# Kernel optimization log

Measured on AMD Instinct MI355X. Metric: run time of the kernel, lower is better.

## Reference

```python
import jax, jax.numpy as jnp
import numpy as np

DIM = 768
NUM_HEADS = 12
HEAD_DIM = DIM // NUM_HEADS
SCALE = HEAD_DIM ** -0.5


def setup_inputs() -> dict:
    key = jax.random.key(0)
    k_x, k_qkv, k_proj, k_pb = jax.random.split(key, 4)
    B, N, C = 16, 1024, DIM
    x = jax.random.normal(k_x, (B, N, C), dtype=jnp.float32)
    # qkv Linear: weight [3C, C], no bias (qkv_bias=False)
    w_qkv = jax.random.normal(k_qkv, (3 * C, C), dtype=jnp.float32) * (C ** -0.5)
    # proj Linear: weight [C, C], bias [C]
    w_proj = jax.random.normal(k_proj, (C, C), dtype=jnp.float32) * (C ** -0.5)
    b_proj = jax.random.normal(k_pb, (C,), dtype=jnp.float32) * 0.01
    return {"x": x, "w_qkv": w_qkv, "w_proj": w_proj, "b_proj": b_proj}


def reference(x, w_qkv, w_proj, b_proj):
    B, N, C = x.shape
    H, D = NUM_HEADS, HEAD_DIM
    # qkv projection: [B,N,3C] -> [3,B,H,N,D]
    qkv = jnp.einsum('bnc,ec->bne', x, w_qkv)
    qkv = qkv.reshape(B, N, 3, H, D).transpose(2, 0, 3, 1, 4)
    q, k, v = qkv[0], qkv[1], qkv[2]
    # manual attention: scores [B,H,N,N] materialized, as in source
    attn = jnp.einsum('bhqd,bhkd->bhqk', q, k) * SCALE
    attn = jax.nn.softmax(attn, axis=-1)
    out = jnp.einsum('bhqk,bhkd->bhqd', attn, v)  # [B,H,N,D]
    out = out.transpose(0, 2, 1, 3).reshape(B, N, C)
    out = jnp.einsum('bnc,oc->bno', out, w_proj) + b_proj
    return out
```

## Files before the change

kernel.cpp:

```cpp
#include <hip/hip_runtime.h>
#include <hip/hip_bf16.h>
#include <stdint.h>

typedef __attribute__((ext_vector_type(8))) short short8;
typedef __attribute__((ext_vector_type(4))) short short4v;
typedef __attribute__((ext_vector_type(4))) float floatx4;

#define B_   16
#define N_   1024
#define C_   768
#define H_   12
#define D_   64
#define K_   768
#define QSCALE 0.18033688011112042f

__device__ __forceinline__ short f2bf(float f) {
    __hip_bfloat16 h = __float2bfloat16(f);
    short s; __builtin_memcpy(&s, &h, 2); return s;
}
__device__ __forceinline__ unsigned pk2bf(float a, float b) {
    __hip_bfloat162 h = __float22bfloat162_rn(make_float2(a, b));
    unsigned u; __builtin_memcpy(&u, &h, 4); return u;
}

__device__ __forceinline__ void gl_lds16(const void* g, void* l) {
    __builtin_amdgcn_global_load_lds(
        (const __attribute__((address_space(1))) unsigned int*)g,
        (__attribute__((address_space(3))) unsigned int*)l, 16, 0, 0);
}

#define N8_X  1572864
#define N8_WQ 221184
#define N8_WP 73728
__global__ void cvt_all(const float* __restrict__ x, const float* __restrict__ wq,
                        const float* __restrict__ wp, short* __restrict__ xb,
                        short* __restrict__ wqb, short* __restrict__ wpb)
{
    long i = (long)blockIdx.x * 256 + threadIdx.x;
    const float* src; short* dst;
    if (i < N8_X)              { src = x;  dst = xb;  }
    else if (i < N8_X + N8_WQ) { src = wq; dst = wqb; i -= N8_X; }
    else                       { src = wp; dst = wpb; i -= (long)N8_X + N8_WQ; }
    const float4* p = (const float4*)src + 2 * i;
    const float4 u = p[0], v = p[1];
    short8 r;
    r[0] = f2bf(u.x); r[1] = f2bf(u.y); r[2] = f2bf(u.z); r[3] = f2bf(u.w);
    r[4] = f2bf(v.x); r[5] = f2bf(v.y); r[6] = f2bf(v.z); r[7] = f2bf(v.w);
    *((short8*)dst + i) = r;
}

template<int MODE>
__global__ __launch_bounds__(256, 3)
void gemm_bt(const short* __restrict__ A, const short* __restrict__ Bm,
             const float* __restrict__ bias,
             short* __restrict__ q_ws, short* __restrict__ k_ws,
             short* __restrict__ v_ws, float* __restrict__ outp)
{
    __shared__ short Alds[128 * 32];
    __shared__ short Blds[128 * 32];
    const int tid  = threadIdx.x;
    const int wave = tid >> 6, lane = tid & 63;
    const int cl   = lane & 15, quad = lane >> 4;
    const int bm = blockIdx.x, bn = blockIdx.y;
    const int wm = (wave >> 1) * 64, wn = (wave & 1) * 64;

    const short* Ag = A  + (long)bm * 128 * K_ + (long)(tid >> 2) * K_ + (tid & 3) * 8;
    const short* Bg = Bm + (long)bn * 128 * K_ + (long)(tid >> 2) * K_ + (tid & 3) * 8;
    short* la = Alds + (tid & 0xC0) * 8;
    short* lb = Blds + (tid & 0xC0) * 8;

    const floatx4 fzero = {0.f, 0.f, 0.f, 0.f};
    floatx4 acc[4][4];
    #pragma unroll
    for (int i = 0; i < 4; i++)
        #pragma unroll
        for (int j = 0; j < 4; j++) acc[i][j] = fzero;

    for (int kt = 0; kt < K_; kt += 32) {
        __syncthreads();
        gl_lds16(Ag + kt,            la);
        gl_lds16(Ag + kt + 64 * K_,  la + 2048);
        gl_lds16(Bg + kt,            lb);
        gl_lds16(Bg + kt + 64 * K_,  lb + 2048);
        __syncthreads();

        short8 af[4], bf[4];
        #pragma unroll
        for (int i = 0; i < 4; i++)
            af[i] = *(const short8*)(Alds + (wm + i * 16 + cl) * 32 + quad * 8);
        #pragma unroll
        for (int j = 0; j < 4; j++)
            bf[j] = *(const short8*)(Blds + (wn + j * 16 + cl) * 32 + quad * 8);
        #pragma unroll
        for (int i = 0; i < 4; i++)
            #pragma unroll
            for (int j = 0; j < 4; j++)
                acc[i][j] = __builtin_amdgcn_mfma_f32_16x16x32_bf16(af[i], bf[j], acc[i][j], 0, 0, 0);
    }

    #pragma unroll
    for (int i = 0; i < 4; i++) {
        const int gm0 = bm * 128 + wm + i * 16 + quad * 4;
        #pragma unroll
        for (int j = 0; j < 4; j++) {
            const int gn = bn * 128 + wn + j * 16 + cl;
            if (MODE == 0) {
                const int t   = bn / 6;
                const int rem = gn - t * 768;
                const int h   = rem >> 6, d = rem & 63;
                const int b   = gm0 >> 10;
                const int n0  = gm0 & 1023;
                const int bh  = b * H_ + h;
                if (t == 2) {
                    short4v pk;
                    #pragma unroll
                    for (int r = 0; r < 4; r++) pk[r] = f2bf(acc[i][j][r]);
                    *(short4v*)(v_ws + (((long)(bh * D_ + d)) << 10) + n0) = pk;
                } else {
                    short* dst = (t == 0) ? q_ws : k_ws;
                    const float sc = (t == 0) ? QSCALE : 1.0f;
                    #pragma unroll
                    for (int r = 0; r < 4; r++)
                        dst[((long)bh * N_ + (n0 + r)) * D_ + d] = f2bf(acc[i][j][r] * sc);
                }
            } else {
                const float bv = bias[gn];
                #pragma unroll
                for (int r = 0; r < 4; r++)
                    outp[(long)(gm0 + r) * C_ + gn] = acc[i][j][r] + bv;
            }
        }
    }
}

__global__ __launch_bounds__(256, 3)
void attn_fused(const short* __restrict__ q_ws, const short* __restrict__ k_ws,
                const short* __restrict__ v_ws, short* __restrict__ o_ws)
{
    __shared__ short Klds[128 * 72];
    __shared__ short Vlds[64 * 136];
    __shared__ short Plds[4][16 * 136];

    const int tid  = threadIdx.x;
    const int wave = tid >> 6, lane = tid & 63;
    const int cl   = lane & 15, quad = lane >> 4;

    const int linear = blockIdx.y * 8 + blockIdx.x;
    const int xcd = linear & 7, slot = linear >> 3;
    const int bh  = xcd * 24 + (slot >> 3);
    const int qt  = slot & 7;

    const long base = (long)bh * (N_ * D_);
    const int  qr0  = qt * 128 + wave * 32 + cl;

    short8 qf[2][2];
    #pragma unroll
    for (int mt = 0; mt < 2; mt++) {
        qf[mt][0] = *(const short8*)(q_ws + base + (long)(qr0 + mt * 16) * D_ + quad * 8);
        qf[mt][1] = *(const short8*)(q_ws + base + (long)(qr0 + mt * 16) * D_ + 32 + quad * 8);
    }

    const floatx4 fzero = {0.f, 0.f, 0.f, 0.f};
    float m_r[2][4], l_r[2][4];
    floatx4 o_acc[2][4];
    #pragma unroll
    for (int mt = 0; mt < 2; mt++)
        #pragma unroll
        for (int r = 0; r < 4; r++) {
            m_r[mt][r] = -1e30f; l_r[mt][r] = 0.f; o_acc[mt][r] = fzero;
        }

    const int skey = tid >> 3, sseg = (tid & 7) * 8;
    const int vd   = tid >> 4, vc = tid & 15;
    short* pl = &Plds[wave][0];

    for (int kc = 0; kc < N_; kc += 128) {
        short8 kst[4], vst[4];
        #pragma unroll
        for (int p = 0; p < 4; p++) {
            kst[p] = *(const short8*)(k_ws + base + (long)(kc + p * 32 + skey) * D_ + sseg);
            #pragma unroll
            for (int i = 0; i < 8; i++)
                vst[p][i] = v_ws[base + (long)(p * 16 + vd) * N_ + kc + i * 16 + vc];
        }
        __syncthreads();
        #pragma unroll
        for (int p = 0; p < 4; p++) {
            *(short8*)(Klds + (p * 32 + skey) * 72 + sseg) = kst[p];
            *(short8*)(Vlds + (p * 16 + vd) * 136 + vc * 8) = vst[p];
        }
        __syncthreads();

        #pragma unroll
        for (int mt = 0; mt < 2; mt++) {
            floatx4 s[8];
            #pragma unroll
            for (int nt = 0; nt < 8; nt++) {
                short8 kf0 = *(const short8*)(Klds + (nt * 16 + cl) * 72 + quad * 8);
                short8 kf1 = *(const short8*)(Klds + (nt * 16 + cl) * 72 + 32 + quad * 8);
                floatx4 t4 = fzero;
                t4 = __builtin_amdgcn_mfma_f32_16x16x32_bf16(qf[mt][0], kf0, t4, 0, 0, 0);
                t4 = __builtin_amdgcn_mfma_f32_16x16x32_bf16(qf[mt][1], kf1, t4, 0, 0, 0);
                s[nt] = t4;
            }

            float alpha[4];
            #pragma unroll
            for (int r = 0; r < 4; r++) {
                float v = s[0][r];
                #pragma unroll
                for (int nt = 1; nt < 8; nt++) v = fmaxf(v, s[nt][r]);
                v = fmaxf(v, __shfl_xor(v, 1));
                v = fmaxf(v, __shfl_xor(v, 2));
                v = fmaxf(v, __shfl_xor(v, 4));
                v = fmaxf(v, __shfl_xor(v, 8));
                const float mn = fmaxf(m_r[mt][r], v);
                alpha[r] = __builtin_amdgcn_exp2f(m_r[mt][r] - mn);
                m_r[mt][r] = mn;
                l_r[mt][r] *= alpha[r];
            }
            #pragma unroll
            for (int r = 0; r < 4; r++) {
                float p0 = __builtin_amdgcn_exp2f(s[0][r] - m_r[mt][r]);
                float p1 = __builtin_amdgcn_exp2f(s[1][r] - m_r[mt][r]);
                float p2 = __builtin_amdgcn_exp2f(s[2][r] - m_r[mt][r]);
                float p3 = __builtin_amdgcn_exp2f(s[3][r] - m_r[mt][r]);
                float p4 = __builtin_amdgcn_exp2f(s[4][r] - m_r[mt][r]);
                float p5 = __builtin_amdgcn_exp2f(s[5][r] - m_r[mt][r]);
                float p6 = __builtin_amdgcn_exp2f(s[6][r] - m_r[mt][r]);
                float p7 = __builtin_amdgcn_exp2f(s[7][r] - m_r[mt][r]);
                l_r[mt][r] += ((p0 + p1) + (p2 + p3)) + ((p4 + p5) + (p6 + p7));
                uint4 pk = { pk2bf(p0, p1), pk2bf(p2, p3), pk2bf(p4, p5), pk2bf(p6, p7) };
                *(uint4*)(pl + (quad * 4 + r) * 136 + cl * 8) = pk;
            }
            #pragma unroll
            for (int dt = 0; dt < 4; dt++) {
                o_acc[mt][dt][0] *= alpha[0]; o_acc[mt][dt][1] *= alpha[1];
                o_acc[mt][dt][2] *= alpha[2]; o_acc[mt][dt][3] *= alpha[3];
            }
            asm volatile("" ::: "memory");

            #pragma unroll
            for (int ks = 0; ks < 4; ks++) {
                short8 pf = *(const short8*)(pl + cl * 136 + ks * 32 + quad * 8);
                #pragma unroll
                for (int dt = 0; dt < 4; dt++) {
                    short8 vf = *(const short8*)(Vlds + (dt * 16 + cl) * 136 + ks * 32 + quad * 8);
                    o_acc[mt][dt] = __builtin_amdgcn_mfma_f32_16x16x32_bf16(pf, vf, o_acc[mt][dt], 0, 0, 0);
                }
            }
            asm volatile("" ::: "memory");
        }
    }

    const int b = bh / H_, h = bh - b * H_;
    #pragma unroll
    for (int mt = 0; mt < 2; mt++) {
        #pragma unroll
        for (int r = 0; r < 4; r++) {
            float v = l_r[mt][r];
            v += __shfl_xor(v, 1); v += __shfl_xor(v, 2);
            v += __shfl_xor(v, 4); v += __shfl_xor(v, 8);
            l_r[mt][r] = 1.0f / v;
        }
        const int nrow = qt * 128 + wave * 32 + mt * 16 + quad * 4;
        #pragma unroll
        for (int dt = 0; dt < 4; dt++) {
            const int c = h * D_ + dt * 16 + cl;
            #pragma unroll
            for (int r = 0; r < 4; r++)
                o_ws[((long)(b * N_ + nrow + r)) * C_ + c] = f2bf(o_acc[mt][dt][r] * l_r[mt][r]);
        }
    }
}

extern "C" void kernel_launch(void* const* d_in, const int* in_sizes, int n_in,
                              void* d_out, int out_size, void* d_ws, size_t ws_size,
                              hipStream_t stream)
{
    const float* x      = (const float*)d_in[0];
    const float* w_qkv  = (const float*)d_in[1];
    const float* w_proj = (const float*)d_in[2];
    const float* b_proj = (const float*)d_in[3];
    float* out = (float*)d_out;

    const long SZ = (long)B_ * N_ * C_;
    short* q_ws   = (short*)d_ws;
    short* k_ws   = q_ws + SZ;
    short* v_ws   = k_ws + SZ;
    short* x_bf   = v_ws + SZ;
    short* o_ws   = x_bf;
    short* wqkv_bf  = x_bf + SZ;
    short* wproj_bf = wqkv_bf + (long)3 * C_ * C_;

    cvt_all<<<dim3(7296), 256, 0, stream>>>(x, w_qkv, w_proj, x_bf, wqkv_bf, wproj_bf);
    gemm_bt<0><<<dim3(128, 18), 256, 0, stream>>>(x_bf, wqkv_bf, nullptr, q_ws, k_ws, v_ws, nullptr);
    attn_fused<<<dim3(8, 192), 256, 0, stream>>>(q_ws, k_ws, v_ws, o_ws);
    gemm_bt<1><<<dim3(128, 6), 256, 0, stream>>>(o_ws, wproj_bf, b_proj, nullptr, nullptr, nullptr, out);
}
```

Before: 313.2 us.

## Shrink attention KV tile to 64, swizzle LDS, and permute V workspace layout

```diff
diff --git a/kernel.cpp b/kernel.cpp
--- a/kernel.cpp
+++ b/kernel.cpp
@@ -112,10 +112,12 @@
                 const int n0  = gm0 & 1023;
                 const int bh  = b * H_ + h;
                 if (t == 2) {
-                    short4v pk;
                     #pragma unroll
-                    for (int r = 0; r < 4; r++) pk[r] = f2bf(acc[i][j][r]);
-                    *(short4v*)(v_ws + (((long)(bh * D_ + d)) << 10) + n0) = pk;
+                    for (int r = 0; r < 4; r++) {
+                        const int n = n0 + r, w = n & 63;
+                        const int vn = (n & ~63) | (((w & 15) << 2) | (w >> 4));
+                        v_ws[(((long)(bh * D_ + d)) << 10) + vn] = f2bf(acc[i][j][r]);
+                    }
                 } else {
                     short* dst = (t == 0) ? q_ws : k_ws;
                     const float sc = (t == 0) ? QSCALE : 1.0f;
@@ -133,13 +135,13 @@
     }
 }
 
-__global__ __launch_bounds__(256, 3)
+__global__ __launch_bounds__(256, 6)
 void attn_fused(const short* __restrict__ q_ws, const short* __restrict__ k_ws,
                 const short* __restrict__ v_ws, short* __restrict__ o_ws)
 {
-    __shared__ short Klds[128 * 72];
-    __shared__ short Vlds[64 * 136];
-    __shared__ short Plds[4][16 * 136];
+    __shared__ short Klds[64 * 64];
+    __shared__ short Vlds[64 * 64];
+    __shared__ short Plds[4][16 * 72];
 
     const int tid  = threadIdx.x;
     const int wave = tid >> 6, lane = tid & 63;
@@ -170,34 +172,32 @@
             m_r[mt][r] = -1e30f; l_r[mt][r] = 0.f; o_acc[mt][r] = fzero;
         }
 
-    const int skey = tid >> 3, sseg = (tid & 7) * 8;
-    const int vd   = tid >> 4, vc = tid & 15;
+    const int srow = tid >> 2;
+    const int sg0  = (tid & 3) * 2;
+    const int xw   = srow & 7;
+    const int xr   = cl & 7;
     short* pl = &Plds[wave][0];
 
-    for (int kc = 0; kc < N_; kc += 128) {
-        short8 kst[4], vst[4];
-        #pragma unroll
-        for (int p = 0; p < 4; p++) {
-            kst[p] = *(const short8*)(k_ws + base + (long)(kc + p * 32 + skey) * D_ + sseg);
-            #pragma unroll
-            for (int i = 0; i < 8; i++)
-                vst[p][i] = v_ws[base + (long)(p * 16 + vd) * N_ + kc + i * 16 + vc];
-        }
-        __syncthreads();
-        #pragma unroll
-        for (int p = 0; p < 4; p++) {
-            *(short8*)(Klds + (p * 32 + skey) * 72 + sseg) = kst[p];
-            *(short8*)(Vlds + (p * 16 + vd) * 136 + vc * 8) = vst[p];
-        }
+    for (int kc = 0; kc < N_; kc += 64) {
+        short8 k0 = *(const short8*)(k_ws + base + (long)(kc + srow) * D_ + sg0 * 8);
+        short8 k1 = *(const short8*)(k_ws + base + (long)(kc + srow) * D_ + sg0 * 8 + 8);
+        short8 v0 = *(const short8*)(v_ws + base + (long)srow * N_ + kc + sg0 * 8);
+        short8 v1 = *(const short8*)(v_ws + base + (long)srow * N_ + kc + sg0 * 8 + 8);
+        __syncthreads();
+        *(short8*)(Klds + srow * 64 + ((sg0    ) ^ xw) * 8) = k0;
+        *(short8*)(Klds + srow * 64 + ((sg0 + 1) ^ xw) * 8) = k1;
+        *(short8*)(Vlds + srow * 64 + ((sg0    ) ^ xw) * 8) = v0;
+        *(short8*)(Vlds + srow * 64 + ((sg0 + 1) ^ xw) * 8) = v1;
         __syncthreads();
 
         #pragma unroll
         for (int mt = 0; mt < 2; mt++) {
-            floatx4 s[8];
-            #pragma unroll
-            for (int nt = 0; nt < 8; nt++) {
-                short8 kf0 = *(const short8*)(Klds + (nt * 16 + cl) * 72 + quad * 8);
-                short8 kf1 = *(const short8*)(Klds + (nt * 16 + cl) * 72 + 32 + quad * 8);
+            floatx4 s[4];
+            #pragma unroll
+            for (int nt = 0; nt < 4; nt++) {
+                const short* kr = Klds + (nt * 16 + cl) * 64;
+                short8 kf0 = *(const short8*)(kr + ((quad    ) ^ xr) * 8);
+                short8 kf1 = *(const short8*)(kr + ((quad + 4) ^ xr) * 8);
                 floatx4 t4 = fzero;
                 t4 = __builtin_amdgcn_mfma_f32_16x16x32_bf16(qf[mt][0], kf0, t4, 0, 0, 0);
                 t4 = __builtin_amdgcn_mfma_f32_16x16x32_bf16(qf[mt][1], kf1, t4, 0, 0, 0);
@@ -207,9 +207,7 @@
             float alpha[4];
             #pragma unroll
             for (int r = 0; r < 4; r++) {
-                float v = s[0][r];
-                #pragma unroll
-                for (int nt = 1; nt < 8; nt++) v = fmaxf(v, s[nt][r]);
+                float v = fmaxf(fmaxf(s[0][r], s[1][r]), fmaxf(s[2][r], s[3][r]));
                 v = fmaxf(v, __shfl_xor(v, 1));
                 v = fmaxf(v, __shfl_xor(v, 2));
                 v = fmaxf(v, __shfl_xor(v, 4));
@@ -225,13 +223,9 @@
                 float p1 = __builtin_amdgcn_exp2f(s[1][r] - m_r[mt][r]);
                 float p2 = __builtin_amdgcn_exp2f(s[2][r] - m_r[mt][r]);
                 float p3 = __builtin_amdgcn_exp2f(s[3][r] - m_r[mt][r]);
-                float p4 = __builtin_amdgcn_exp2f(s[4][r] - m_r[mt][r]);
-                float p5 = __builtin_amdgcn_exp2f(s[5][r] - m_r[mt][r]);
-                float p6 = __builtin_amdgcn_exp2f(s[6][r] - m_r[mt][r]);
-                float p7 = __builtin_amdgcn_exp2f(s[7][r] - m_r[mt][r]);
-                l_r[mt][r] += ((p0 + p1) + (p2 + p3)) + ((p4 + p5) + (p6 + p7));
-                uint4 pk = { pk2bf(p0, p1), pk2bf(p2, p3), pk2bf(p4, p5), pk2bf(p6, p7) };
-                *(uint4*)(pl + (quad * 4 + r) * 136 + cl * 8) = pk;
+                l_r[mt][r] += (p0 + p1) + (p2 + p3);
+                uint2 pk = { pk2bf(p0, p1), pk2bf(p2, p3) };
+                *(uint2*)(pl + (quad * 4 + r) * 72 + cl * 4) = pk;
             }
             #pragma unroll
             for (int dt = 0; dt < 4; dt++) {
@@ -241,11 +235,12 @@
             asm volatile("" ::: "memory");
 
             #pragma unroll
-            for (int ks = 0; ks < 4; ks++) {
-                short8 pf = *(const short8*)(pl + cl * 136 + ks * 32 + quad * 8);
+            for (int ks = 0; ks < 2; ks++) {
+                short8 pf = *(const short8*)(pl + cl * 72 + ks * 32 + quad * 8);
                 #pragma unroll
                 for (int dt = 0; dt < 4; dt++) {
-                    short8 vf = *(const short8*)(Vlds + (dt * 16 + cl) * 136 + ks * 32 + quad * 8);
+                    const short* vr = Vlds + (dt * 16 + cl) * 64;
+                    short8 vf = *(const short8*)(vr + ((ks * 4 + quad) ^ xr) * 8);
                     o_acc[mt][dt] = __builtin_amdgcn_mfma_f32_16x16x32_bf16(pf, vf, o_acc[mt][dt], 0, 0, 0);
                 }
             }
```

Result: slower. 459.8 us (+46.8%).

## Vectorize V loads, XOR-swizzle K/V LDS, share K fragments across row tiles

Applied to the files above, without the earlier changes.

```diff
diff --git a/kernel.cpp b/kernel.cpp
--- a/kernel.cpp
+++ b/kernel.cpp
@@ -137,8 +137,8 @@
 void attn_fused(const short* __restrict__ q_ws, const short* __restrict__ k_ws,
                 const short* __restrict__ v_ws, short* __restrict__ o_ws)
 {
-    __shared__ short Klds[128 * 72];
-    __shared__ short Vlds[64 * 136];
+    __shared__ short Klds[128 * 64];
+    __shared__ short Vlds[64 * 128];
     __shared__ short Plds[4][16 * 136];
 
     const int tid  = threadIdx.x;
@@ -170,46 +170,51 @@
             m_r[mt][r] = -1e30f; l_r[mt][r] = 0.f; o_acc[mt][r] = fzero;
         }
 
-    const int skey = tid >> 3, sseg = (tid & 7) * 8;
-    const int vd   = tid >> 4, vc = tid & 15;
+    const int skey = tid >> 3, sseg = tid & 7;
+    const int vd   = tid >> 4, vseg = tid & 15;
     short* pl = &Plds[wave][0];
 
     for (int kc = 0; kc < N_; kc += 128) {
         short8 kst[4], vst[4];
         #pragma unroll
         for (int p = 0; p < 4; p++) {
-            kst[p] = *(const short8*)(k_ws + base + (long)(kc + p * 32 + skey) * D_ + sseg);
-            #pragma unroll
-            for (int i = 0; i < 8; i++)
-                vst[p][i] = v_ws[base + (long)(p * 16 + vd) * N_ + kc + i * 16 + vc];
+            kst[p] = *(const short8*)(k_ws + base + (long)(kc + p * 32 + skey) * D_ + sseg * 8);
+            vst[p] = *(const short8*)(v_ws + base + (long)(p * 16 + vd) * N_ + kc + vseg * 8);
         }
         __syncthreads();
         #pragma unroll
         for (int p = 0; p < 4; p++) {
-            *(short8*)(Klds + (p * 32 + skey) * 72 + sseg) = kst[p];
-            *(short8*)(Vlds + (p * 16 + vd) * 136 + vc * 8) = vst[p];
+            const int krow = p * 32 + skey;
+            const int fk   = ((krow >> 3) ^ (krow & 7)) & 7;
+            *(short8*)(Klds + krow * 64 + (sseg ^ fk) * 8) = kst[p];
+            const int vrow = p * 16 + vd;
+            *(short8*)(Vlds + vrow * 128 + (vseg ^ (vrow & 7)) * 8) = vst[p];
         }
         __syncthreads();
 
+        floatx4 s[2][8];
+        #pragma unroll
+        for (int nt = 0; nt < 8; nt++) {
+            const int krow = cl * 8 + nt;
+            const int fk   = ((krow >> 3) ^ (krow & 7)) & 7;
+            const short* kr = Klds + krow * 64;
+            short8 kf0 = *(const short8*)(kr + ((quad    ) ^ fk) * 8);
+            short8 kf1 = *(const short8*)(kr + ((quad + 4) ^ fk) * 8);
+            floatx4 t0 = fzero, t1 = fzero;
+            t0 = __builtin_amdgcn_mfma_f32_16x16x32_bf16(qf[0][0], kf0, t0, 0, 0, 0);
+            t0 = __builtin_amdgcn_mfma_f32_16x16x32_bf16(qf[0][1], kf1, t0, 0, 0, 0);
+            t1 = __builtin_amdgcn_mfma_f32_16x16x32_bf16(qf[1][0], kf0, t1, 0, 0, 0);
+            t1 = __builtin_amdgcn_mfma_f32_16x16x32_bf16(qf[1][1], kf1, t1, 0, 0, 0);
+            s[0][nt] = t0; s[1][nt] = t1;
+        }
+
         #pragma unroll
         for (int mt = 0; mt < 2; mt++) {
-            floatx4 s[8];
-            #pragma unroll
-            for (int nt = 0; nt < 8; nt++) {
-                short8 kf0 = *(const short8*)(Klds + (nt * 16 + cl) * 72 + quad * 8);
-                short8 kf1 = *(const short8*)(Klds + (nt * 16 + cl) * 72 + 32 + quad * 8);
-                floatx4 t4 = fzero;
-                t4 = __builtin_amdgcn_mfma_f32_16x16x32_bf16(qf[mt][0], kf0, t4, 0, 0, 0);
-                t4 = __builtin_amdgcn_mfma_f32_16x16x32_bf16(qf[mt][1], kf1, t4, 0, 0, 0);
-                s[nt] = t4;
-            }
-
             float alpha[4];
             #pragma unroll
             for (int r = 0; r < 4; r++) {
-                float v = s[0][r];
-                #pragma unroll
-                for (int nt = 1; nt < 8; nt++) v = fmaxf(v, s[nt][r]);
+                float v = fmaxf(fmaxf(s[mt][0][r], s[mt][1][r]), fmaxf(s[mt][2][r], s[mt][3][r]));
+                v = fmaxf(v, fmaxf(fmaxf(s[mt][4][r], s[mt][5][r]), fmaxf(s[mt][6][r], s[mt][7][r])));
                 v = fmaxf(v, __shfl_xor(v, 1));
                 v = fmaxf(v, __shfl_xor(v, 2));
                 v = fmaxf(v, __shfl_xor(v, 4));
@@ -221,14 +226,14 @@
             }
             #pragma unroll
             for (int r = 0; r < 4; r++) {
-                float p0 = __builtin_amdgcn_exp2f(s[0][r] - m_r[mt][r]);
-                float p1 = __builtin_amdgcn_exp2f(s[1][r] - m_r[mt][r]);
-                float p2 = __builtin_amdgcn_exp2f(s[2][r] - m_r[mt][r]);
-                float p3 = __builtin_amdgcn_exp2f(s[3][r] - m_r[mt][r]);
-                float p4 = __builtin_amdgcn_exp2f(s[4][r] - m_r[mt][r]);
-                float p5 = __builtin_amdgcn_exp2f(s[5][r] - m_r[mt][r]);
-                float p6 = __builtin_amdgcn_exp2f(s[6][r] - m_r[mt][r]);
-                float p7 = __builtin_amdgcn_exp2f(s[7][r] - m_r[mt][r]);
+                float p0 = __builtin_amdgcn_exp2f(s[mt][0][r] - m_r[mt][r]);
+                float p1 = __builtin_amdgcn_exp2f(s[mt][1][r] - m_r[mt][r]);
+                float p2 = __builtin_amdgcn_exp2f(s[mt][2][r] - m_r[mt][r]);
+                float p3 = __builtin_amdgcn_exp2f(s[mt][3][r] - m_r[mt][r]);
+                float p4 = __builtin_amdgcn_exp2f(s[mt][4][r] - m_r[mt][r]);
+                float p5 = __builtin_amdgcn_exp2f(s[mt][5][r] - m_r[mt][r]);
+                float p6 = __builtin_amdgcn_exp2f(s[mt][6][r] - m_r[mt][r]);
+                float p7 = __builtin_amdgcn_exp2f(s[mt][7][r] - m_r[mt][r]);
                 l_r[mt][r] += ((p0 + p1) + (p2 + p3)) + ((p4 + p5) + (p6 + p7));
                 uint4 pk = { pk2bf(p0, p1), pk2bf(p2, p3), pk2bf(p4, p5), pk2bf(p6, p7) };
                 *(uint4*)(pl + (quad * 4 + r) * 136 + cl * 8) = pk;
@@ -245,7 +250,9 @@
                 short8 pf = *(const short8*)(pl + cl * 136 + ks * 32 + quad * 8);
                 #pragma unroll
                 for (int dt = 0; dt < 4; dt++) {
-                    short8 vf = *(const short8*)(Vlds + (dt * 16 + cl) * 136 + ks * 32 + quad * 8);
+                    const int vrow = dt * 16 + cl;
+                    const short* vr = Vlds + vrow * 128;
+                    short8 vf = *(const short8*)(vr + ((ks * 4 + quad) ^ (vrow & 7)) * 8);
                     o_acc[mt][dt] = __builtin_amdgcn_mfma_f32_16x16x32_bf16(pf, vf, o_acc[mt][dt], 0, 0, 0);
                 }
             }
```

Result: faster. 304.1 us (-2.9%).
